# Optimization experiments

Hardware: AMD Instinct MI355X
Metric: run time of the kernel (lower is better)

Reference implementation:

```python
import jax, jax.numpy as jnp
import numpy as np

T, S, F, A, P = 64, 32, 256, 64, 32  # t, s, feature_len, attn_len, posembed_len


def setup_inputs() -> dict:
    key = jax.random.key(0)
    ks = jax.random.split(key, 8)
    w = lambda k, shape: jax.random.normal(k, shape, dtype=jnp.float32) * 0.02
    return {
        "batch_data": jax.random.normal(ks[0], (T * S, F), dtype=jnp.float32),
        "positions": jax.random.normal(ks[1], (2, S, S, 9), dtype=jnp.float32),
        "temp": jax.random.normal(ks[2], (T, T, S, 10), dtype=jnp.float32),
        "Wa": w(ks[3], (F, A)), "ba": jnp.zeros((A,), jnp.float32),
        "Wb": w(ks[4], (F + 2 * P, A)), "bb": jnp.zeros((A,), jnp.float32),
        "Wg": w(ks[5], (F + 2 * P, F)), "bg": jnp.zeros((F,), jnp.float32),
        "Wpos": w(ks[6], (9, P)), "bpos": jnp.zeros((P,), jnp.float32),
        "Wtmp": w(ks[7], (10, 2 * P)), "btmp": jnp.zeros((2 * P,), jnp.float32),
    }


def reference(batch_data, positions, temp, Wa, ba, Wb, bb, Wg, bg, Wpos, bpos, Wtmp, btmp):
    x = batch_data.reshape(T, S, F)                      # (T,S,F)
    # pairwise spatial embedding: pos[j,k] used for query node j, key node k
    pos = jnp.concatenate([positions[0] @ Wpos + bpos,
                           positions[1] @ Wpos + bpos], axis=-1)  # (S,S,2P)
    tmp = temp @ Wtmp + btmp                              # (T,T,S,2P)
    theta = x @ Wa + ba                                   # (T,S,A)

    # Linear on concat([x, p]) == x @ W[:F] + p @ W[F:] + b; split to avoid
    # materializing the broadcast concatenated tensor.
    WbX, WbP = Wb[:F], Wb[F:]
    WgX, WgP = Wg[:F], Wg[F:]
    x_phi = x @ WbX                                       # (T,S,A)
    x_g = x @ WgX                                         # (T,S,F)

    # ---- spatial pass: keys over nodes k at same time ----
    phi_s = x_phi[None] + (pos @ WbP)[:, None] + bb       # (Sq,T,Sk,A)
    feat_s = x_g[None] + (pos @ WgP)[:, None] + bg        # (Sq,T,Sk,F)
    scores_s = jnp.einsum('ija,jika->ijk', theta, phi_s)  # (T,Sq,Sk)
    attn_s = jax.nn.softmax(scores_s, axis=-1)
    res = jnp.einsum('ijk,jikf->ijf', attn_s, feat_s)     # (T,S,F)

    # ---- temporal pass: keys over times tau at same node ----
    phi_t = x_phi[None] + tmp @ WbP + bb                  # (Tq,T,S,A)
    feat_t = x_g[None] + tmp @ WgP + bg                   # (Tq,T,S,F)
    scores_t = jnp.einsum('jia,jtia->jit', theta, phi_t)  # (Tq,S,Tk)
    attn_t = jax.nn.softmax(scores_t, axis=-1)
    res = res + jnp.einsum('jit,jtif->jif', attn_t, feat_t)
    return res                                            # (T,S,F)
```

## Files before the change

kernel.cpp:

```cpp
#include <hip/hip_runtime.h>

constexpr int T = 64, S = 32, F = 256, A = 64;
constexpr int R = T * S;

constexpr size_t OFF_XPH = 0;
constexpr size_t OFF_TH  = OFF_XPH + (size_t)R * A;
constexpr size_t OFF_UU  = OFF_TH  + (size_t)R * A;
constexpr size_t OFF_DD  = OFF_UU  + (size_t)R * A;
constexpr size_t OFF_POS = OFF_DD  + (size_t)R * 16;

__device__ __forceinline__ float dot4(float4 a, float4 b) {
    return a.x * b.x + a.y * b.y + a.z * b.z + a.w * b.w;
}
__device__ __forceinline__ float4 f4fma(float s, float4 v, float4 a) {
    a.x += s * v.x; a.y += s * v.y; a.z += s * v.z; a.w += s * v.w; return a;
}
__device__ __forceinline__ float4 f4add(float4 a, float4 b) {
    a.x += b.x; a.y += b.y; a.z += b.z; a.w += b.w; return a;
}

__global__ __launch_bounds__(256) void k_pre(
    const float* __restrict__ bd, const float* __restrict__ Wa,
    const float* __restrict__ ba, const float* __restrict__ Wb,
    const float* __restrict__ Wtmp, const float* __restrict__ positions,
    const float* __restrict__ Wpos, const float* __restrict__ bpos,
    float* __restrict__ xph, float* __restrict__ th,
    float* __restrict__ uu, float* __restrict__ dd, float* __restrict__ pos)
{
    const int blk = blockIdx.x;
    const int tid = threadIdx.x;

    if (blk >= 256) {
        const int idx = (blk - 256) * 256 + tid;
        const int p = idx & 63, jk = idx >> 6;
        const int e = p >> 5, pp = p & 31;
        const float* src = positions + (size_t)(e * 1024 + jk) * 9;
        float acc = bpos[pp];
#pragma unroll
        for (int q = 0; q < 9; ++q) acc += src[q] * Wpos[q * 32 + pp];
        pos[idx] = acc;
        return;
    }

    __shared__ float xs[8 * 256];
    __shared__ float ths[8][64];
    __shared__ float us[8][64];
    const int w = tid >> 6, lane = tid & 63;
    const int row0 = blk * 8 + 2 * w;

    {
        const float4* src = (const float4*)(bd + (size_t)blk * 8 * 256);
        float4* dst = (float4*)xs;
        dst[tid] = src[tid];
        dst[tid + 256] = src[tid + 256];
    }
    __syncthreads();

    const float* x0 = xs + (2 * w) * 256;
    const float* x1 = xs + (2 * w + 1) * 256;
    float accA0 = ba[lane], accA1 = accA0, accB0 = 0.f, accB1 = 0.f;
#pragma unroll
    for (int c0 = 0; c0 < 256; c0 += 8) {
        float wa[8], wb[8];
#pragma unroll
        for (int j = 0; j < 8; ++j) wa[j] = Wa[(c0 + j) * 64 + lane];
#pragma unroll
        for (int j = 0; j < 8; ++j) wb[j] = Wb[(c0 + j) * 64 + lane];
#pragma unroll
        for (int j = 0; j < 8; ++j) {
            const float xa = x0[c0 + j], xb = x1[c0 + j];
            accA0 += xa * wa[j]; accA1 += xb * wa[j];
            accB0 += xa * wb[j]; accB1 += xb * wb[j];
        }
    }
    th[(size_t)row0 * 64 + lane] = accA0;
    th[(size_t)(row0 + 1) * 64 + lane] = accA1;
    xph[(size_t)row0 * 64 + lane] = accB0;
    xph[(size_t)(row0 + 1) * 64 + lane] = accB1;
    ths[2 * w][lane] = accA0; ths[2 * w + 1][lane] = accA1;
    __syncthreads();

    float accU0 = 0.f, accU1 = 0.f;
#pragma unroll 8
    for (int a = 0; a < 64; ++a) {
        const float wp = Wb[(256 + lane) * 64 + a];
        accU0 += ths[2 * w][a] * wp;
        accU1 += ths[2 * w + 1][a] * wp;
    }
    uu[(size_t)row0 * 64 + lane] = accU0;
    uu[(size_t)(row0 + 1) * 64 + lane] = accU1;
    us[2 * w][lane] = accU0; us[2 * w + 1][lane] = accU1;
    __syncthreads();

    const int rsel = lane >> 4, q = lane & 15;
    if (rsel < 2 && q < 10) {
        float accD = 0.f;
#pragma unroll 8
        for (int p2 = 0; p2 < 64; ++p2) accD += us[2 * w + rsel][p2] * Wtmp[q * 64 + p2];
        dd[(size_t)(row0 + rsel) * 16 + q] = accD;
    }
}

__global__ __launch_bounds__(256) void k_fuse(
    const float* __restrict__ bd, const float* __restrict__ temp,
    const float* __restrict__ Wtmp, const float* __restrict__ btmp,
    const float* __restrict__ Wg, const float* __restrict__ bg,
    const float* __restrict__ xph, const float* __restrict__ th,
    const float* __restrict__ uu, const float* __restrict__ dd,
    const float* __restrict__ pos, float* __restrict__ out)
{
    const int ss = blockIdx.x >> 4;
    const int tt0 = (blockIdx.x & 15) * 4;
    const int tid = threadIdx.x;
    const int w = tid >> 6, lane = tid & 63;

    __shared__ float th_s[4][64], u_s[4][64], d_s[4][16];
    __shared__ float es[4][32], et[4][64], w10[4][10];
    __shared__ float zz[4][320];
    __shared__ float4 part4[4][4][64];

    {
        const size_t r = (size_t)(tt0 + w) * 32 + ss;
        th_s[w][lane] = th[r * 64 + lane];
        u_s[w][lane]  = uu[r * 64 + lane];
        if (lane < 16) d_s[w][lane] = dd[r * 16 + lane];
    }
    __syncthreads();

    {
        const int t = lane;
        const float4* xp = (const float4*)(xph + ((size_t)t * 32 + ss) * 64);
        const float4* tv4 = (const float4*)th_s[w];
        float sc = 0.f;
#pragma unroll
        for (int a = 0; a < 16; ++a) sc += dot4(xp[a], tv4[a]);
        const float2* tp = (const float2*)(temp + (((size_t)(tt0 + w) * 64 + t) * 32 + ss) * 10);
        const float2* dv = (const float2*)d_s[w];
        float2 tmpv[5];
#pragma unroll
        for (int q = 0; q < 5; ++q) {
            tmpv[q] = tp[q];
            const float2 d2 = dv[q];
            sc += tmpv[q].x * d2.x + tmpv[q].y * d2.y;
        }
        float m = sc;
#pragma unroll
        for (int off = 32; off; off >>= 1) m = fmaxf(m, __shfl_xor(m, off));
        const float e = __expf(sc - m);
        float s = e;
#pragma unroll
        for (int off = 32; off; off >>= 1) s += __shfl_xor(s, off);
        const float at = e / s;
        et[w][t] = at;
        float r10[10];
#pragma unroll
        for (int q = 0; q < 5; ++q) { r10[2 * q] = at * tmpv[q].x; r10[2 * q + 1] = at * tmpv[q].y; }
#pragma unroll
        for (int off = 32; off; off >>= 1) {
#pragma unroll
            for (int i = 0; i < 10; ++i) r10[i] += __shfl_xor(r10[i], off);
        }
        if (lane == 0) {
#pragma unroll
            for (int i = 0; i < 10; ++i) w10[w][i] = r10[i];
        }
    }

    if (tid < 128) {
        const int ttl = tid >> 5, k = tid & 31;
        const float4* xp = (const float4*)(xph + ((size_t)(tt0 + ttl) * 32 + k) * 64);
        const float4* pp = (const float4*)(pos + ((size_t)ss * 32 + k) * 64);
        const float4* tv4 = (const float4*)th_s[ttl];
        const float4* uv4 = (const float4*)u_s[ttl];
        float sc = 0.f;
#pragma unroll
        for (int a = 0; a < 16; ++a) sc += dot4(xp[a], tv4[a]) + dot4(pp[a], uv4[a]);
        float m = sc;
#pragma unroll
        for (int off = 16; off; off >>= 1) m = fmaxf(m, __shfl_xor(m, off));
        const float e = __expf(sc - m);
        float s = e;
#pragma unroll
        for (int off = 16; off; off >>= 1) s += __shfl_xor(s, off);
        es[ttl][k] = e / s;
    }
    __syncthreads();

    {
        const int p = lane;
        const float* pb = pos + (size_t)ss * 32 * 64 + p;
        float pv = 0.f;
#pragma unroll
        for (int k0 = 0; k0 < 32; k0 += 8) {
            float yv[8];
#pragma unroll
            for (int j = 0; j < 8; ++j) yv[j] = pb[(size_t)(k0 + j) * 64];
#pragma unroll
            for (int j = 0; j < 8; ++j) pv += es[w][k0 + j] * yv[j];
        }
        float g = pv + btmp[p];
#pragma unroll
        for (int q = 0; q < 10; ++q) g += w10[w][q] * Wtmp[q * 64 + p];
        zz[w][256 + p] = g;
    }

    {
        const float4* bd4 = (const float4*)bd;
        float4 acc[4];
#pragma unroll
        for (int r = 0; r < 4; ++r) acc[r] = make_float4(0.f, 0.f, 0.f, 0.f);
#pragma unroll
        for (int j = 0; j < 16; ++j) {
            const int t = 16 * w + j;
            const float4 x4 = bd4[((size_t)t * 32 + ss) * 64 + lane];
#pragma unroll
            for (int r = 0; r < 4; ++r) acc[r] = f4fma(et[r][t], x4, acc[r]);
        }
#pragma unroll
        for (int r = 0; r < 4; ++r) part4[w][r][lane] = acc[r];
    }
    __syncthreads();

    {
        const float4* bd4 = (const float4*)bd;
        float4 a = make_float4(0.f, 0.f, 0.f, 0.f);
#pragma unroll
        for (int k = 0; k < 32; ++k) {
            const float4 x4 = bd4[((size_t)(tt0 + w) * 32 + k) * 64 + lane];
            a = f4fma(es[w][k], x4, a);
        }
#pragma unroll
        for (int w2 = 0; w2 < 4; ++w2) a = f4add(a, part4[w2][w][lane]);
        ((float4*)&zz[w][0])[lane] = a;
    }
    __syncthreads();

    {
        const float4* Wg4 = (const float4*)Wg;
        float4 acc[4];
#pragma unroll
        for (int r = 0; r < 4; ++r) acc[r] = make_float4(0.f, 0.f, 0.f, 0.f);
        const int kbase = 80 * w;
#pragma unroll 4
        for (int j = 0; j < 20; ++j) {
            const int k0 = kbase + 4 * j;
            float4 wg[4];
#pragma unroll
            for (int q = 0; q < 4; ++q) wg[q] = Wg4[(size_t)(k0 + q) * 64 + lane];
#pragma unroll
            for (int r = 0; r < 4; ++r) {
                const float4 zv = *(const float4*)&zz[r][k0];
                acc[r] = f4fma(zv.x, wg[0], acc[r]);
                acc[r] = f4fma(zv.y, wg[1], acc[r]);
                acc[r] = f4fma(zv.z, wg[2], acc[r]);
                acc[r] = f4fma(zv.w, wg[3], acc[r]);
            }
        }
#pragma unroll
        for (int r = 0; r < 4; ++r) part4[w][r][lane] = acc[r];
    }
    __syncthreads();

    {
        float4 o = part4[0][w][lane];
        o = f4add(o, part4[1][w][lane]);
        o = f4add(o, part4[2][w][lane]);
        o = f4add(o, part4[3][w][lane]);
        const float4 b4 = ((const float4*)bg)[lane];
        o.x += 2.f * b4.x; o.y += 2.f * b4.y; o.z += 2.f * b4.z; o.w += 2.f * b4.w;
        ((float4*)out)[((size_t)(tt0 + w) * 32 + ss) * 64 + lane] = o;
    }
}

extern "C" void kernel_launch(void* const* d_in, const int* in_sizes, int n_in,
                              void* d_out, int out_size, void* d_ws, size_t ws_size,
                              hipStream_t stream) {
    const float* bd   = (const float*)d_in[0];
    const float* positions = (const float*)d_in[1];
    const float* temp = (const float*)d_in[2];
    const float* Wa   = (const float*)d_in[3];
    const float* ba   = (const float*)d_in[4];
    const float* Wb   = (const float*)d_in[5];
    const float* Wg   = (const float*)d_in[7];
    const float* bg   = (const float*)d_in[8];
    const float* Wpos = (const float*)d_in[9];
    const float* bpos = (const float*)d_in[10];
    const float* Wtmp = (const float*)d_in[11];
    const float* btmp = (const float*)d_in[12];
    float* out = (float*)d_out;

    float* ws  = (float*)d_ws;
    float* xph = ws + OFF_XPH;
    float* th  = ws + OFF_TH;
    float* uu  = ws + OFF_UU;
    float* dd  = ws + OFF_DD;
    float* pos = ws + OFF_POS;

    k_pre<<<512, 256, 0, stream>>>(bd, Wa, ba, Wb, Wtmp, positions, Wpos, bpos,
                                   xph, th, uu, dd, pos);
    k_fuse<<<512, 256, 0, stream>>>(bd, temp, Wtmp, btmp, Wg, bg,
                                    xph, th, uu, dd, pos, out);
}
```

Before: 116.4 us.

## Precompute x@WgX in fp16 and apply attention to projected features

The pre-kernel's second half of blocks now also computes x@Wg[:F] for all rows and stores it in half precision. The fused kernel applies the attention weights directly to these projected rows, by linearity, instead of to raw x. Only the 64-row positional part of Wg is still multiplied per block, which removes the large 320x256 per-block GEMM and halves the bytes gathered. The cost is extra work in the pre-kernel and fp16 rounding error in the gathered features.

```diff
diff --git a/kernel.cpp b/kernel.cpp
--- a/kernel.cpp
+++ b/kernel.cpp
@@ -1,4 +1,5 @@
 #include <hip/hip_runtime.h>
+#include <hip/hip_fp16.h>
 
 constexpr int T = 64, S = 32, F = 256, A = 64;
 constexpr int R = T * S;
@@ -8,6 +9,7 @@
 constexpr size_t OFF_UU  = OFF_TH  + (size_t)R * A;
 constexpr size_t OFF_DD  = OFF_UU  + (size_t)R * A;
 constexpr size_t OFF_POS = OFF_DD  + (size_t)R * 16;
+constexpr size_t OFF_XGH = OFF_POS + (size_t)S * S * 64;
 
 __device__ __forceinline__ float dot4(float4 a, float4 b) {
     return a.x * b.x + a.y * b.y + a.z * b.z + a.w * b.w;
@@ -17,34 +19,69 @@
 }
 __device__ __forceinline__ float4 f4add(float4 a, float4 b) {
     a.x += b.x; a.y += b.y; a.z += b.z; a.w += b.w; return a;
+}
+__device__ __forceinline__ float4 ldh4(const __half* p, size_t idx4) {
+    float2 raw = ((const float2*)p)[idx4];
+    const __half2* h = reinterpret_cast<const __half2*>(&raw);
+    const float2 lo = __half22float2(h[0]);
+    const float2 hi = __half22float2(h[1]);
+    return make_float4(lo.x, lo.y, hi.x, hi.y);
 }
 
 __global__ __launch_bounds__(256) void k_pre(
     const float* __restrict__ bd, const float* __restrict__ Wa,
     const float* __restrict__ ba, const float* __restrict__ Wb,
-    const float* __restrict__ Wtmp, const float* __restrict__ positions,
-    const float* __restrict__ Wpos, const float* __restrict__ bpos,
+    const float* __restrict__ Wg, const float* __restrict__ Wtmp,
+    const float* __restrict__ positions, const float* __restrict__ Wpos,
+    const float* __restrict__ bpos,
     float* __restrict__ xph, float* __restrict__ th,
-    float* __restrict__ uu, float* __restrict__ dd, float* __restrict__ pos)
+    float* __restrict__ uu, float* __restrict__ dd,
+    float* __restrict__ pos, __half* __restrict__ XG_h)
 {
     const int blk = blockIdx.x;
     const int tid = threadIdx.x;
 
-    if (blk >= 256) {
-        const int idx = (blk - 256) * 256 + tid;
-        const int p = idx & 63, jk = idx >> 6;
-        const int e = p >> 5, pp = p & 31;
-        const float* src = positions + (size_t)(e * 1024 + jk) * 9;
-        float acc = bpos[pp];
-#pragma unroll
-        for (int q = 0; q < 9; ++q) acc += src[q] * Wpos[q * 32 + pp];
-        pos[idx] = acc;
-        return;
-    }
-
     __shared__ float xs[8 * 256];
     __shared__ float ths[8][64];
     __shared__ float us[8][64];
+
+    if (blk >= 256) {
+        const int xb = blk - 256;
+        {
+            const int idx = xb * 256 + tid;
+            const int p = idx & 63, jk = idx >> 6;
+            const int e = p >> 5, pp = p & 31;
+            const float* src = positions + (size_t)(e * 1024 + jk) * 9;
+            float acc = bpos[pp];
+#pragma unroll
+            for (int q = 0; q < 9; ++q) acc += src[q] * Wpos[q * 32 + pp];
+            pos[idx] = acc;
+        }
+        {
+            const float4* src = (const float4*)(bd + (size_t)xb * 8 * 256);
+            float4* dst = (float4*)xs;
+            dst[tid] = src[tid];
+            dst[tid + 256] = src[tid + 256];
+        }
+        __syncthreads();
+        float acc[8] = {0.f, 0.f, 0.f, 0.f, 0.f, 0.f, 0.f, 0.f};
+#pragma unroll
+        for (int c0 = 0; c0 < 256; c0 += 8) {
+            float wv[8];
+#pragma unroll
+            for (int j = 0; j < 8; ++j) wv[j] = Wg[(size_t)(c0 + j) * 256 + tid];
+#pragma unroll
+            for (int j = 0; j < 8; ++j) {
+#pragma unroll
+                for (int r = 0; r < 8; ++r) acc[r] += xs[r * 256 + c0 + j] * wv[j];
+            }
+        }
+#pragma unroll
+        for (int r = 0; r < 8; ++r)
+            XG_h[(size_t)(xb * 8 + r) * 256 + tid] = __float2half(acc[r]);
+        return;
+    }
+
     const int w = tid >> 6, lane = tid & 63;
     const int row0 = blk * 8 + 2 * w;
 
@@ -68,9 +105,9 @@
         for (int j = 0; j < 8; ++j) wb[j] = Wb[(c0 + j) * 64 + lane];
 #pragma unroll
         for (int j = 0; j < 8; ++j) {
-            const float xa = x0[c0 + j], xb = x1[c0 + j];
-            accA0 += xa * wa[j]; accA1 += xb * wa[j];
-            accB0 += xa * wb[j]; accB1 += xb * wb[j];
+            const float xa = x0[c0 + j], xb2 = x1[c0 + j];
+            accA0 += xa * wa[j]; accA1 += xb2 * wa[j];
+            accB0 += xa * wb[j]; accB1 += xb2 * wb[j];
         }
     }
     th[(size_t)row0 * 64 + lane] = accA0;
@@ -102,12 +139,12 @@
 }
 
 __global__ __launch_bounds__(256) void k_fuse(
-    const float* __restrict__ bd, const float* __restrict__ temp,
-    const float* __restrict__ Wtmp, const float* __restrict__ btmp,
-    const float* __restrict__ Wg, const float* __restrict__ bg,
-    const float* __restrict__ xph, const float* __restrict__ th,
-    const float* __restrict__ uu, const float* __restrict__ dd,
-    const float* __restrict__ pos, float* __restrict__ out)
+    const float* __restrict__ temp, const float* __restrict__ Wtmp,
+    const float* __restrict__ btmp, const float* __restrict__ Wg,
+    const float* __restrict__ bg, const float* __restrict__ xph,
+    const float* __restrict__ th, const float* __restrict__ uu,
+    const float* __restrict__ dd, const float* __restrict__ pos,
+    const __half* __restrict__ XG_h, float* __restrict__ out)
 {
     const int ss = blockIdx.x >> 4;
     const int tt0 = (blockIdx.x & 15) * 4;
@@ -116,8 +153,10 @@
 
     __shared__ float th_s[4][64], u_s[4][64], d_s[4][16];
     __shared__ float es[4][32], et[4][64], w10[4][10];
-    __shared__ float zz[4][320];
+    __shared__ float gs[4][64];
+    __shared__ float4 zz4[4][64];
     __shared__ float4 part4[4][4][64];
+    __shared__ float4 part4b[4][4][64];
 
     {
         const size_t r = (size_t)(tt0 + w) * 32 + ss;
@@ -201,18 +240,17 @@
         float g = pv + btmp[p];
 #pragma unroll
         for (int q = 0; q < 10; ++q) g += w10[w][q] * Wtmp[q * 64 + p];
-        zz[w][256 + p] = g;
-    }
-
-    {
-        const float4* bd4 = (const float4*)bd;
+        gs[w][p] = g;
+    }
+
+    {
         float4 acc[4];
 #pragma unroll
         for (int r = 0; r < 4; ++r) acc[r] = make_float4(0.f, 0.f, 0.f, 0.f);
 #pragma unroll
         for (int j = 0; j < 16; ++j) {
             const int t = 16 * w + j;
-            const float4 x4 = bd4[((size_t)t * 32 + ss) * 64 + lane];
+            const float4 x4 = ldh4(XG_h, ((size_t)t * 32 + ss) * 64 + lane);
 #pragma unroll
             for (int r = 0; r < 4; ++r) acc[r] = f4fma(et[r][t], x4, acc[r]);
         }
@@ -222,50 +260,38 @@
     __syncthreads();
 
     {
-        const float4* bd4 = (const float4*)bd;
         float4 a = make_float4(0.f, 0.f, 0.f, 0.f);
 #pragma unroll
         for (int k = 0; k < 32; ++k) {
-            const float4 x4 = bd4[((size_t)(tt0 + w) * 32 + k) * 64 + lane];
+            const float4 x4 = ldh4(XG_h, ((size_t)(tt0 + w) * 32 + k) * 64 + lane);
             a = f4fma(es[w][k], x4, a);
         }
 #pragma unroll
         for (int w2 = 0; w2 < 4; ++w2) a = f4add(a, part4[w2][w][lane]);
-        ((float4*)&zz[w][0])[lane] = a;
-    }
-    __syncthreads();
-
+        zz4[w][lane] = a;
+    }
     {
         const float4* Wg4 = (const float4*)Wg;
         float4 acc[4];
 #pragma unroll
         for (int r = 0; r < 4; ++r) acc[r] = make_float4(0.f, 0.f, 0.f, 0.f);
-        const int kbase = 80 * w;
-#pragma unroll 4
-        for (int j = 0; j < 20; ++j) {
-            const int k0 = kbase + 4 * j;
-            float4 wg[4];
-#pragma unroll
-            for (int q = 0; q < 4; ++q) wg[q] = Wg4[(size_t)(k0 + q) * 64 + lane];
-#pragma unroll
-            for (int r = 0; r < 4; ++r) {
-                const float4 zv = *(const float4*)&zz[r][k0];
-                acc[r] = f4fma(zv.x, wg[0], acc[r]);
-                acc[r] = f4fma(zv.y, wg[1], acc[r]);
-                acc[r] = f4fma(zv.z, wg[2], acc[r]);
-                acc[r] = f4fma(zv.w, wg[3], acc[r]);
-            }
-        }
-#pragma unroll
-        for (int r = 0; r < 4; ++r) part4[w][r][lane] = acc[r];
-    }
-    __syncthreads();
-
-    {
-        float4 o = part4[0][w][lane];
-        o = f4add(o, part4[1][w][lane]);
-        o = f4add(o, part4[2][w][lane]);
-        o = f4add(o, part4[3][w][lane]);
+#pragma unroll
+        for (int j = 0; j < 16; ++j) {
+            const int pp = 16 * w + j;
+            const float4 wg = Wg4[(size_t)(256 + pp) * 64 + lane];
+#pragma unroll
+            for (int r = 0; r < 4; ++r) acc[r] = f4fma(gs[r][pp], wg, acc[r]);
+        }
+#pragma unroll
+        for (int r = 0; r < 4; ++r) part4b[w][r][lane] = acc[r];
+    }
+    __syncthreads();
+
+    {
+        float4 o = f4add(zz4[w][lane], part4b[0][w][lane]);
+        o = f4add(o, part4b[1][w][lane]);
+        o = f4add(o, part4b[2][w][lane]);
+        o = f4add(o, part4b[3][w][lane]);
         const float4 b4 = ((const float4*)bg)[lane];
         o.x += 2.f * b4.x; o.y += 2.f * b4.y; o.z += 2.f * b4.z; o.w += 2.f * b4.w;
         ((float4*)out)[((size_t)(tt0 + w) * 32 + ss) * 64 + lane] = o;
@@ -295,9 +321,10 @@
     float* uu  = ws + OFF_UU;
     float* dd  = ws + OFF_DD;
     float* pos = ws + OFF_POS;
-
-    k_pre<<<512, 256, 0, stream>>>(bd, Wa, ba, Wb, Wtmp, positions, Wpos, bpos,
-                                   xph, th, uu, dd, pos);
-    k_fuse<<<512, 256, 0, stream>>>(bd, temp, Wtmp, btmp, Wg, bg,
-                                    xph, th, uu, dd, pos, out);
-}
+    __half* XG_h = (__half*)(ws + OFF_XGH);
+
+    k_pre<<<512, 256, 0, stream>>>(bd, Wa, ba, Wb, Wg, Wtmp, positions, Wpos,
+                                   bpos, xph, th, uu, dd, pos, XG_h);
+    k_fuse<<<512, 256, 0, stream>>>(temp, Wtmp, btmp, Wg, bg,
+                                    xph, th, uu, dd, pos, XG_h, out);
+}
```

Result: faster. 111.0 us (-4.6%).
